# Performance work log

Measured on AMD Instinct MI355X. Metric: run time of the kernel, lower is better.

The kernel has to match this reference:

```python
import jax, jax.numpy as jnp
import numpy as np

N = 100000   # nodes
E = 1600000  # edges per view
B = 256      # graphs in batch
D = 128      # feature dim
H, C = 4, 32 # heads, per-head channels (H*C = 128)


def _seg_softmax(logits, seg, num_seg):
    # numerically stable softmax over segments (per-destination / per-graph)
    m = jax.ops.segment_max(logits, seg, num_segments=num_seg)
    e = jnp.exp(logits - m[seg])
    s = jax.ops.segment_sum(e, seg, num_segments=num_seg)
    return e / s[seg]


def _gat_conv(x, edge_index, W, att_src, att_dst, bias):
    # PyG GATConv with add_self_loops=True, concat heads
    n = x.shape[0]
    loop = jnp.arange(n, dtype=edge_index.dtype)
    src = jnp.concatenate([edge_index[0], loop])
    dst = jnp.concatenate([edge_index[1], loop])
    xh = (x @ W).reshape(n, H, C)                      # [N,H,C]
    a_src = jnp.einsum('nhc,hc->nh', xh, att_src)      # [N,H]
    a_dst = jnp.einsum('nhc,hc->nh', xh, att_dst)
    alpha = jax.nn.leaky_relu(a_src[src] + a_dst[dst], 0.2)   # [E+N,H]
    alpha = _seg_softmax(alpha, dst, n)
    msg = xh[src] * alpha[..., None]                   # [E+N,H,C]
    out = jax.ops.segment_sum(msg, dst, num_segments=n)
    return out.reshape(n, H * C) + bias


def _global_attention(h, batch, gate_W, gate_b):
    gate = (h @ gate_W + gate_b)[:, 0]                 # [N]
    a = _seg_softmax(gate, batch, B)
    return jax.ops.segment_sum(a[:, None] * h, batch, num_segments=B)  # [B,128]


def setup_inputs() -> dict:
    key = jax.random.key(0)
    ks = jax.random.split(key, 32)
    p = lambda k, shp: (jax.random.normal(k, shp, dtype=jnp.float32) * 0.05)
    inp = {
        'x': jax.random.normal(ks[0], (N, D), dtype=jnp.float32),
        'edge_index_ast': jax.random.randint(ks[1], (2, E), 0, N, dtype=jnp.int32),
        'edge_index_cfg': jax.random.randint(ks[2], (2, E), 0, N, dtype=jnp.int32),
        'edge_index_pdg': jax.random.randint(ks[3], (2, E), 0, N, dtype=jnp.int32),
        'batch': jnp.sort(jax.random.randint(ks[4], (N,), 0, B, dtype=jnp.int32)),
        'ln_g': jnp.ones((D,), jnp.float32),
        'ln_b': jnp.zeros((D,), jnp.float32),
        'proj_W': p(ks[5], (D, D)), 'proj_b': p(ks[6], (D,)),
        'W_ast': p(ks[7], (D, H * C)), 'att_src_ast': p(ks[8], (H, C)), 'att_dst_ast': p(ks[9], (H, C)), 'bias_ast': p(ks[10], (H * C,)),
        'W_cfg': p(ks[11], (D, H * C)), 'att_src_cfg': p(ks[12], (H, C)), 'att_dst_cfg': p(ks[13], (H, C)), 'bias_cfg': p(ks[14], (H * C,)),
        'W_pdg': p(ks[15], (D, H * C)), 'att_src_pdg': p(ks[16], (H, C)), 'att_dst_pdg': p(ks[17], (H, C)), 'bias_pdg': p(ks[18], (H * C,)),
        'gate_W': p(ks[19], (H * C, 1)), 'gate_b': p(ks[20], (1,)),
        'clf_W1': p(ks[21], (3 * H * C, 128)), 'clf_b1': p(ks[22], (128,)),
        'clf_W2': p(ks[23], (128, 1)), 'clf_b2': p(ks[24], (1,)),
    }
    return inp


def reference(x, edge_index_ast, edge_index_cfg, edge_index_pdg, batch,
              ln_g, ln_b, proj_W, proj_b,
              W_ast, att_src_ast, att_dst_ast, bias_ast,
              W_cfg, att_src_cfg, att_dst_cfg, bias_cfg,
              W_pdg, att_src_pdg, att_dst_pdg, bias_pdg,
              gate_W, gate_b, clf_W1, clf_b1, clf_W2, clf_b2):
    # LayerNorm + proj + LeakyReLU (dropout = eval/no-op)
    mu = jnp.mean(x, axis=-1, keepdims=True)
    var = jnp.var(x, axis=-1, keepdims=True)
    xn = (x - mu) * jax.lax.rsqrt(var + 1e-5) * ln_g + ln_b
    h0 = jax.nn.leaky_relu(xn @ proj_W + proj_b, 0.01)

    h_ast = jax.nn.elu(_gat_conv(h0, edge_index_ast, W_ast, att_src_ast, att_dst_ast, bias_ast))
    g_ast = _global_attention(h_ast, batch, gate_W, gate_b)
    h_cfg = jax.nn.elu(_gat_conv(h0, edge_index_cfg, W_cfg, att_src_cfg, att_dst_cfg, bias_cfg))
    g_cfg = _global_attention(h_cfg, batch, gate_W, gate_b)
    h_pdg = jax.nn.elu(_gat_conv(h0, edge_index_pdg, W_pdg, att_src_pdg, att_dst_pdg, bias_pdg))
    g_pdg = _global_attention(h_pdg, batch, gate_W, gate_b)

    combined = jnp.concatenate([g_ast, g_cfg, g_pdg], axis=1)  # [B, 384]
    hid = jax.nn.leaky_relu(combined @ clf_W1 + clf_b1, 0.01)
    return (hid @ clf_W2 + clf_b2).reshape(-1)                 # [B]
```

## Files before the change

### kernel.cpp

```cpp
#include <hip/hip_runtime.h>
#include <hip/hip_bf16.h>
#include <hip/hip_fp16.h>
#include <math.h>

#define NN 100000
#define EE 1600000
#define BB 256
#define NBUCK 391
#define PBLK 384
#define CH 4167
#define TOTB (3 * PBLK)
#define ROWS_PAD 100096
#define SCAP 4608
#define OBCAP (SCAP + 256)
#define LOG2E 1.442695041f
#define GEMM_BLKS 782
#define AGG_BLKS 25000
#define EPT 17
#define XH_ELEMS ((size_t)ROWS_PAD * 128)
#define A_ELEMS ((size_t)ROWS_PAD * 4)
#define HV_ELEMS ((size_t)NN * 128)

typedef short bf16x8 __attribute__((ext_vector_type(8)));
typedef float f32x4 __attribute__((ext_vector_type(4)));

__device__ __forceinline__ unsigned short f2bf(float f) {
    __hip_bfloat16 h = __float2bfloat16(f);
    return *(unsigned short*)&h;
}
__device__ __forceinline__ unsigned short f2h(float f) {
    __half h = __float2half(f);
    return *(unsigned short*)&h;
}
__device__ __forceinline__ float h2f(unsigned short u) {
    __half h = *(__half*)&u;
    return __half2float(h);
}

__global__ __launch_bounds__(256) void prep_kernel(const float* __restrict__ W0,
                                                   const float* __restrict__ W1,
                                                   const float* __restrict__ W2,
                                                   const float* __restrict__ W3,
                                                   const float* __restrict__ ln_g,
                                                   const float* __restrict__ ln_b,
                                                   unsigned short* __restrict__ WT,
                                                   float* __restrict__ c12,
                                                   int* __restrict__ counters) {
    if (blockIdx.x < 256) {
        int which = blockIdx.x >> 6;
        const float* W = which == 0 ? W0 : which == 1 ? W1 : which == 2 ? W2 : W3;
        int i = (blockIdx.x & 63) * 256 + threadIdx.x;
        int n = i >> 7, k = i & 127;
        float v = W[k * 128 + n];
        if (which == 0) v *= ln_g[k];
        WT[which * 16384 + i] = f2bf(v);
        return;
    }
    if (blockIdx.x == 257) {
        for (int i = threadIdx.x; i < 3 * NBUCK; i += 256) counters[i] = 0;
        return;
    }
    __shared__ float p1[256], p2[256];
    int t = threadIdx.x;
    int n = t & 127, kg = t >> 7;
    float c1 = 0.f, c2 = 0.f;
    for (int k = kg * 64; k < kg * 64 + 64; k++) {
        float w = W0[k * 128 + n];
        c1 = fmaf(ln_g[k], w, c1);
        c2 = fmaf(ln_b[k], w, c2);
    }
    p1[t] = c1; p2[t] = c2;
    __syncthreads();
    if (kg == 0) {
        c12[n] = p1[n] + p1[128 + n];
        c12[128 + n] = p2[n] + p2[128 + n];
    }
}


__device__ __forceinline__ void scatter_res_body(int bid, int tid,
                                                 const int* __restrict__ e0,
                                                 const int* __restrict__ e1,
                                                 const int* __restrict__ e2,
                                                 int* __restrict__ counters,
                                                 unsigned int* __restrict__ pairbuf) {
    int v = bid / PBLK, p = bid % PBLK;
    const int* ei = v == 0 ? e0 : v == 1 ? e1 : e2;
    __shared__ int hcnt[NBUCK];
    __shared__ int cur[NBUCK];
    for (int i = tid; i < NBUCK; i += 256) hcnt[i] = 0;
    __syncthreads();
    int ea = p * CH, ebnd = min(EE, ea + CH);
    unsigned val[EPT];
    int buck[EPT];
    #pragma unroll
    for (int k = 0; k < EPT; k++) {
        int e = ea + tid + k * 256;
        buck[k] = -1;
        val[k] = 0u;
        if (e < ebnd) {
            unsigned s = (unsigned)ei[e], d = (unsigned)ei[EE + e];
            val[k] = (s << 8) | (d & 255u);
            buck[k] = (int)(d >> 8);
        }
    }
    #pragma unroll
    for (int k = 0; k < EPT; k++)
        if (buck[k] >= 0) atomicAdd(&hcnt[buck[k]], 1);
    __syncthreads();
    int* gcnt = counters + v * NBUCK;
    for (int i = tid; i < NBUCK; i += 256) {
        int c = hcnt[i];
        cur[i] = c ? atomicAdd(&gcnt[i], c) : 0;
    }
    __syncthreads();
    unsigned int* pbuf = pairbuf + (size_t)v * NBUCK * SCAP;
    #pragma unroll
    for (int k = 0; k < EPT; k++) {
        if (buck[k] >= 0) {
            int pos = atomicAdd(&cur[buck[k]], 1);
            if (pos < SCAP) pbuf[(size_t)buck[k] * SCAP + pos] = val[k];
        }
    }
}

__device__ __forceinline__ void proj_body(int nb, int tid,
                                          const float* __restrict__ X,
                                          const unsigned short* __restrict__ WT,
                                          const float* __restrict__ c12,
                                          const float* __restrict__ pb,
                                          unsigned short* __restrict__ Out) {
    int w = tid >> 6, lane = tid & 63;
    int ln = lane & 15, oct = lane >> 4;
    int row0 = nb * 128 + w * 32;

    f32x4 acc[2][8];
    #pragma unroll
    for (int i = 0; i < 2; i++)
        #pragma unroll
        for (int j = 0; j < 8; j++) acc[i][j] = (f32x4){0.f, 0.f, 0.f, 0.f};

    const float* X0 = X + (size_t)min(row0 + ln, NN - 1) * 128;
    const float* X1 = X + (size_t)min(row0 + 16 + ln, NN - 1) * 128;
    const bf16x8* Wr = (const bf16x8*)(WT + (size_t)ln * 128);

    float s0 = 0.f, q0 = 0.f, s1 = 0.f, q1 = 0.f;
    #pragma unroll
    for (int kq = 0; kq < 4; kq++) {
        int koff = kq * 4 + oct;
        float4 xa = *(const float4*)(X0 + koff * 8);
        float4 xb = *(const float4*)(X0 + koff * 8 + 4);
        float4 ya = *(const float4*)(X1 + koff * 8);
        float4 yb = *(const float4*)(X1 + koff * 8 + 4);
        s0 += (xa.x + xa.y) + (xa.z + xa.w) + (xb.x + xb.y) + (xb.z + xb.w);
        q0 += xa.x * xa.x + xa.y * xa.y + xa.z * xa.z + xa.w * xa.w
            + xb.x * xb.x + xb.y * xb.y + xb.z * xb.z + xb.w * xb.w;
        s1 += (ya.x + ya.y) + (ya.z + ya.w) + (yb.x + yb.y) + (yb.z + yb.w);
        q1 += ya.x * ya.x + ya.y * ya.y + ya.z * ya.z + ya.w * ya.w
            + yb.x * yb.x + yb.y * yb.y + yb.z * yb.z + yb.w * yb.w;
        bf16x8 a0, a1;
        a0[0] = (short)f2bf(xa.x); a0[1] = (short)f2bf(xa.y); a0[2] = (short)f2bf(xa.z); a0[3] = (short)f2bf(xa.w);
        a0[4] = (short)f2bf(xb.x); a0[5] = (short)f2bf(xb.y); a0[6] = (short)f2bf(xb.z); a0[7] = (short)f2bf(xb.w);
        a1[0] = (short)f2bf(ya.x); a1[1] = (short)f2bf(ya.y); a1[2] = (short)f2bf(ya.z); a1[3] = (short)f2bf(ya.w);
        a1[4] = (short)f2bf(yb.x); a1[5] = (short)f2bf(yb.y); a1[6] = (short)f2bf(yb.z); a1[7] = (short)f2bf(yb.w);
        #pragma unroll
        for (int ct = 0; ct < 8; ct++) {
            bf16x8 bfr = Wr[ct * 16 * 16 + koff];
            acc[0][ct] = __builtin_amdgcn_mfma_f32_16x16x32_bf16(a0, bfr, acc[0][ct], 0, 0, 0);
            acc[1][ct] = __builtin_amdgcn_mfma_f32_16x16x32_bf16(a1, bfr, acc[1][ct], 0, 0, 0);
        }
    }
    #pragma unroll
    for (int m = 16; m < 64; m <<= 1) {
        s0 += __shfl_xor(s0, m); q0 += __shfl_xor(q0, m);
        s1 += __shfl_xor(s1, m); q1 += __shfl_xor(q1, m);
    }
    float mu0 = s0 * (1.0f / 128.0f);
    float rs0 = rsqrtf(q0 * (1.0f / 128.0f) - mu0 * mu0 + 1e-5f);
    float mu1 = s1 * (1.0f / 128.0f);
    float rs1 = rsqrtf(q1 * (1.0f / 128.0f) - mu1 * mu1 + 1e-5f);

    float c1v[8], c2v[8], pbv[8];
    #pragma unroll
    for (int ct = 0; ct < 8; ct++) {
        c1v[ct] = c12[ct * 16 + ln];
        c2v[ct] = c12[128 + ct * 16 + ln];
        pbv[ct] = pb[ct * 16 + ln];
    }
    #pragma unroll
    for (int rt = 0; rt < 2; rt++) {
        #pragma unroll
        for (int r = 0; r < 4; r++) {
            int src = oct * 4 + r;
            float rs_r = __shfl(rt ? rs1 : rs0, src);
            float mu_r = __shfl(rt ? mu1 : mu0, src);
            int row = row0 + rt * 16 + oct * 4 + r;
            #pragma unroll
            for (int ct = 0; ct < 8; ct++) {
                float v = rs_r * acc[rt][ct][r] - rs_r * mu_r * c1v[ct] + c2v[ct] + pbv[ct];
                v = v > 0.f ? v : 0.01f * v;
                Out[(size_t)row * 128 + ct * 16 + ln] = f2bf(v);
            }
        }
    }
}

__device__ __forceinline__ void view_body(int nb, int tid,
                                          const unsigned short* __restrict__ h0,
                                          const unsigned short* __restrict__ WTv,
                                          const float* __restrict__ asw,
                                          const float* __restrict__ adw,
                                          unsigned short* __restrict__ Out,
                                          float* __restrict__ a_src,
                                          float* __restrict__ a_dst) {
    int w = tid >> 6, lane = tid & 63;
    int ln = lane & 15, oct = lane >> 4;
    int row0 = nb * 128 + w * 32;

    f32x4 acc[2][8];
    #pragma unroll
    for (int i = 0; i < 2; i++)
        #pragma unroll
        for (int j = 0; j < 8; j++) acc[i][j] = (f32x4){0.f, 0.f, 0.f, 0.f};

    const bf16x8* Ar0 = (const bf16x8*)(h0 + (size_t)(row0 + ln) * 128);
    const bf16x8* Ar1 = (const bf16x8*)(h0 + (size_t)(row0 + 16 + ln) * 128);
    const bf16x8* Wr  = (const bf16x8*)(WTv + (size_t)ln * 128);

    #pragma unroll
    for (int kq = 0; kq < 4; kq++) {
        int koff = kq * 4 + oct;
        bf16x8 a0 = Ar0[koff];
        bf16x8 a1 = Ar1[koff];
        #pragma unroll
        for (int ct = 0; ct < 8; ct++) {
            bf16x8 bfr = Wr[ct * 16 * 16 + koff];
            acc[0][ct] = __builtin_amdgcn_mfma_f32_16x16x32_bf16(a0, bfr, acc[0][ct], 0, 0, 0);
            acc[1][ct] = __builtin_amdgcn_mfma_f32_16x16x32_bf16(a1, bfr, acc[1][ct], 0, 0, 0);
        }
    }
    float aswv[8], adwv[8];
    #pragma unroll
    for (int ct = 0; ct < 8; ct++) {
        aswv[ct] = asw[ct * 16 + ln] * LOG2E;
        adwv[ct] = adw[ct * 16 + ln] * LOG2E;
    }

    #pragma unroll
    for (int rt = 0; rt < 2; rt++) {
        #pragma unroll
        for (int r = 0; r < 4; r++) {
            int row = row0 + rt * 16 + oct * 4 + r;
            float sh_[4] = {0.f, 0.f, 0.f, 0.f}, dh_[4] = {0.f, 0.f, 0.f, 0.f};
            #pragma unroll
            for (int ct = 0; ct < 8; ct++) {
                float vv = acc[rt][ct][r];
                Out[(size_t)row * 128 + ct * 16 + ln] = f2h(vv);
                sh_[ct >> 1] = fmaf(vv, aswv[ct], sh_[ct >> 1]);
                dh_[ct >> 1] = fmaf(vv, adwv[ct], dh_[ct >> 1]);
            }
            #pragma unroll
            for (int off = 1; off < 16; off <<= 1) {
                #pragma unroll
                for (int h = 0; h < 4; h++) {
                    sh_[h] += __shfl_xor(sh_[h], off);
                    dh_[h] += __shfl_xor(dh_[h], off);
                }
            }
            if (ln == 0) {
                *(float4*)(a_src + (size_t)row * 4) = make_float4(sh_[0], sh_[1], sh_[2], sh_[3]);
                *(float4*)(a_dst + (size_t)row * 4) = make_float4(dh_[0], dh_[1], dh_[2], dh_[3]);
            }
        }
    }
}

__device__ __forceinline__ void fine_body(int bid, int t,
                                          const unsigned int* __restrict__ pairbuf,
                                          const int* __restrict__ counters,
                                          int* __restrict__ deg3,
                                          int* __restrict__ start3,
                                          unsigned int* __restrict__ ebuf3) {
    int v = bid / NBUCK, b = bid - v * NBUCK;
    int cnt = min(counters[v * NBUCK + b], SCAP);
    const unsigned int* pb = pairbuf + (size_t)(v * NBUCK + b) * SCAP;
    unsigned int* eb = ebuf3 + (size_t)(v * NBUCK + b) * OBCAP;
    int obase = (v * NBUCK + b) * OBCAP;
    __shared__ unsigned int slab[SCAP];
    __shared__ int hist[256], cur[256];
    __shared__ int wsum[4];
    int node = b * 256 + t;
    int valid = (node < NN) ? 1 : 0;
    hist[t] = valid;
    for (int i = t; i < cnt; i += 256) slab[i] = pb[i];
    __syncthreads();
    {
        int i = t;
        for (; i + 768 < cnt; i += 1024) {
            unsigned v0 = slab[i], v1 = slab[i + 256], v2 = slab[i + 512], v3 = slab[i + 768];
            atomicAdd(&hist[v0 & 255u], 1);
            atomicAdd(&hist[v1 & 255u], 1);
            atomicAdd(&hist[v2 & 255u], 1);
            atomicAdd(&hist[v3 & 255u], 1);
        }
        for (; i < cnt; i += 256) atomicAdd(&hist[slab[i] & 255u], 1);
    }
    __syncthreads();
    int hv = hist[t];
    int lanev = t & 63, wv = t >> 6;
    int incl = hv;
    #pragma unroll
    for (int m = 1; m < 64; m <<= 1) {
        int u = __shfl_up(incl, m);
        if (lanev >= m) incl += u;
    }
    if (lanev == 63) wsum[wv] = incl;
    __syncthreads();
    int prefix = 0;
    #pragma unroll
    for (int i = 0; i < 4; i++) prefix += (i < wv) ? wsum[i] : 0;
    int excl = incl + prefix - hv;
    cur[t] = excl + valid;
    if (valid) eb[excl] = (((unsigned)node) << 8) | ((unsigned)node & 255u);
    __syncthreads();
    {
        int i = t;
        for (; i + 768 < cnt; i += 1024) {
            unsigned v0 = slab[i], v1 = slab[i + 256], v2 = slab[i + 512], v3 = slab[i + 768];
            int p0 = atomicAdd(&cur[v0 & 255u], 1);
            int p1 = atomicAdd(&cur[v1 & 255u], 1);
            int p2 = atomicAdd(&cur[v2 & 255u], 1);
            int p3 = atomicAdd(&cur[v3 & 255u], 1);
            eb[p0] = v0; eb[p1] = v1; eb[p2] = v2; eb[p3] = v3;
        }
        for (; i < cnt; i += 256) {
            unsigned int val = slab[i];
            int pos = atomicAdd(&cur[val & 255u], 1);
            eb[pos] = val;
        }
    }
    if (valid) {
        deg3[v * NN + node] = hv;
        start3[v * NN + node] = obase + excl;
    }
}

__device__ __forceinline__ void agg_body(int node, int tid,
                                         const unsigned short* __restrict__ xh,
                                         const int* __restrict__ start,
                                         const int* __restrict__ deg,
                                         const unsigned int* __restrict__ ebuf,
                                         const float* __restrict__ a_src,
                                         const float* __restrict__ a_dst,
                                         const float* __restrict__ bias,
                                         const float* __restrict__ gw,
                                         const float* __restrict__ gb,
                                         unsigned short* __restrict__ hvb,
                                         float* __restrict__ gexpv,
                                         float* wlds) {
    int lane = tid & 63;
    int h = lane >> 4;
    int st = start[node];
    int cnt = deg[node];
    const char* xb = (const char*)xh;
    int laneoff = lane * 4;
    float4 ad4 = *(const float4*)(a_dst + (size_t)node * 4);
    float* ww = wlds + (tid >> 6) * 272;
    const float* wr = ww + h * 68;

    float accx = 0.f, accy = 0.f, den = 0.f;
    for (int j0 = 0; j0 < cnt; j0 += 64) {
        int nj = min(64, cnt - j0);
        int src_l = 0;
        if (lane < nj) {
            src_l = (int)(ebuf[st + j0 + lane] >> 8);
            float4 as4 = *(const float4*)(a_src + (size_t)src_l * 4);
            float t0 = as4.x + ad4.x, t1 = as4.y + ad4.y;
            float t2 = as4.z + ad4.z, t3 = as4.w + ad4.w;
            t0 = fmaxf(t0, 0.f) + 0.2f * fminf(t0, 0.f);
            t1 = fmaxf(t1, 0.f) + 0.2f * fminf(t1, 0.f);
            t2 = fmaxf(t2, 0.f) + 0.2f * fminf(t2, 0.f);
            t3 = fmaxf(t3, 0.f) + 0.2f * fminf(t3, 0.f);
            ww[0 * 68 + lane] = exp2f(t0);
            ww[1 * 68 + lane] = exp2f(t1);
            ww[2 * 68 + lane] = exp2f(t2);
            ww[3 * 68 + lane] = exp2f(t3);
        }
        int jj = 0;
        for (; jj + 8 <= nj; jj += 8) {
            int s0 = __builtin_amdgcn_readlane(src_l, jj);
            int s1 = __builtin_amdgcn_readlane(src_l, jj + 1);
            int s2 = __builtin_amdgcn_readlane(src_l, jj + 2);
            int s3 = __builtin_amdgcn_readlane(src_l, jj + 3);
            int s4 = __builtin_amdgcn_readlane(src_l, jj + 4);
            int s5 = __builtin_amdgcn_readlane(src_l, jj + 5);
            int s6 = __builtin_amdgcn_readlane(src_l, jj + 6);
            int s7 = __builtin_amdgcn_readlane(src_l, jj + 7);
            __half2 x0 = *(const __half2*)(xb + (((size_t)(unsigned)s0) << 8) + laneoff);
            __half2 x1 = *(const __half2*)(xb + (((size_t)(unsigned)s1) << 8) + laneoff);
            __half2 x2 = *(const __half2*)(xb + (((size_t)(unsigned)s2) << 8) + laneoff);
            __half2 x3 = *(const __half2*)(xb + (((size_t)(unsigned)s3) << 8) + laneoff);
            __half2 x4 = *(const __half2*)(xb + (((size_t)(unsigned)s4) << 8) + laneoff);
            __half2 x5 = *(const __half2*)(xb + (((size_t)(unsigned)s5) << 8) + laneoff);
            __half2 x6 = *(const __half2*)(xb + (((size_t)(unsigned)s6) << 8) + laneoff);
            __half2 x7 = *(const __half2*)(xb + (((size_t)(unsigned)s7) << 8) + laneoff);
            float4 wa = *(const float4*)(wr + jj);
            float4 wb = *(const float4*)(wr + jj + 4);
            den += (wa.x + wa.y) + (wa.z + wa.w) + (wb.x + wb.y) + (wb.z + wb.w);
            accx = fmaf(__low2float(x0), wa.x, accx);
            accy = fmaf(__high2float(x0), wa.x, accy);
            accx = fmaf(__low2float(x1), wa.y, accx);
            accy = fmaf(__high2float(x1), wa.y, accy);
            accx = fmaf(__low2float(x2), wa.z, accx);
            accy = fmaf(__high2float(x2), wa.z, accy);
            accx = fmaf(__low2float(x3), wa.w, accx);
            accy = fmaf(__high2float(x3), wa.w, accy);
            accx = fmaf(__low2float(x4), wb.x, accx);
            accy = fmaf(__high2float(x4), wb.x, accy);
            accx = fmaf(__low2float(x5), wb.y, accx);
            accy = fmaf(__high2float(x5), wb.y, accy);
            accx = fmaf(__low2float(x6), wb.z, accx);
            accy = fmaf(__high2float(x6), wb.z, accy);
            accx = fmaf(__low2float(x7), wb.w, accx);
            accy = fmaf(__high2float(x7), wb.w, accy);
        }
        for (; jj + 4 <= nj; jj += 4) {
            int s0 = __builtin_amdgcn_readlane(src_l, jj);
            int s1 = __builtin_amdgcn_readlane(src_l, jj + 1);
            int s2 = __builtin_amdgcn_readlane(src_l, jj + 2);
            int s3 = __builtin_amdgcn_readlane(src_l, jj + 3);
            __half2 x0 = *(const __half2*)(xb + (((size_t)(unsigned)s0) << 8) + laneoff);
            __half2 x1 = *(const __half2*)(xb + (((size_t)(unsigned)s1) << 8) + laneoff);
            __half2 x2 = *(const __half2*)(xb + (((size_t)(unsigned)s2) << 8) + laneoff);
            __half2 x3 = *(const __half2*)(xb + (((size_t)(unsigned)s3) << 8) + laneoff);
            float4 wa = *(const float4*)(wr + jj);
            den += (wa.x + wa.y) + (wa.z + wa.w);
            accx = fmaf(__low2float(x0), wa.x, accx);
            accy = fmaf(__high2float(x0), wa.x, accy);
            accx = fmaf(__low2float(x1), wa.y, accx);
            accy = fmaf(__high2float(x1), wa.y, accy);
            accx = fmaf(__low2float(x2), wa.z, accx);
            accy = fmaf(__high2float(x2), wa.z, accy);
            accx = fmaf(__low2float(x3), wa.w, accx);
            accy = fmaf(__high2float(x3), wa.w, accy);
        }
        for (; jj < nj; jj++) {
            int s = __builtin_amdgcn_readlane(src_l, jj);
            float w = wr[jj];
            __half2 xv = *(const __half2*)(xb + (((size_t)(unsigned)s) << 8) + laneoff);
            den += w;
            accx = fmaf(__low2float(xv), w, accx);
            accy = fmaf(__high2float(xv), w, accy);
        }
    }
    float inv = 1.0f / den;
    float2 bb = *(const float2*)(bias + lane * 2);
    float o0 = accx * inv + bb.x;
    float o1 = accy * inv + bb.y;
    o0 = o0 > 0.f ? o0 : exp2f(o0 * LOG2E) - 1.0f;
    o1 = o1 > 0.f ? o1 : exp2f(o1 * LOG2E) - 1.0f;
    unsigned int packed = (unsigned)f2h(o0) | ((unsigned)f2h(o1) << 16);
    *(unsigned int*)(hvb + (size_t)node * 128 + lane * 2) = packed;
    float2 g2 = *(const float2*)(gw + lane * 2);
    float gp = o0 * g2.x + o1 * g2.y;
    #pragma unroll
    for (int m = 1; m < 64; m <<= 1) gp += __shfl_xor(gp, m);
    if (lane == 0) gexpv[node] = exp2f((gp + gb[0]) * LOG2E);
}

__global__ __launch_bounds__(256) void fat_scatter_proj(const int* e0, const int* e1, const int* e2,
                                                        int* counters, unsigned int* pairbuf,
                                                        const float* X, const unsigned short* WT,
                                                        const float* c12, const float* pb,
                                                        unsigned short* h0) {
    if (blockIdx.x < TOTB) scatter_res_body(blockIdx.x, threadIdx.x, e0, e1, e2, counters, pairbuf);
    else proj_body(blockIdx.x - TOTB, threadIdx.x, X, WT, c12, pb, h0);
}

__global__ __launch_bounds__(256) void fat_fine_view3(const unsigned int* pairbuf, const int* counters,
                                                      int* deg3, int* start3, unsigned int* ebuf3,
                                                      const unsigned short* h0, const unsigned short* WT,
                                                      const float* as0, const float* ad0,
                                                      const float* as1, const float* ad1,
                                                      const float* as2, const float* ad2,
                                                      unsigned short* xh3, float* a_src3, float* a_dst3) {
    if (blockIdx.x < 3 * NBUCK) {
        fine_body(blockIdx.x, threadIdx.x, pairbuf, counters, deg3, start3, ebuf3);
        return;
    }
    int t = blockIdx.x - 3 * NBUCK;
    int v = t / GEMM_BLKS;
    int nb = t - v * GEMM_BLKS;
    const float* as_ = v == 0 ? as0 : v == 1 ? as1 : as2;
    const float* ad_ = v == 0 ? ad0 : v == 1 ? ad1 : ad2;
    view_body(nb, threadIdx.x, h0, WT + (size_t)(1 + v) * 16384, as_, ad_,
              xh3 + (size_t)v * XH_ELEMS,
              a_src3 + (size_t)v * A_ELEMS, a_dst3 + (size_t)v * A_ELEMS);
}

__global__ __launch_bounds__(256) void aggregate3_kernel(const unsigned short* __restrict__ xh3,
                                                         const int* __restrict__ start3,
                                                         const int* __restrict__ deg3,
                                                         const unsigned int* __restrict__ ebuf3,
                                                         const float* __restrict__ a_src3,
                                                         const float* __restrict__ a_dst3,
                                                         const float* __restrict__ b0,
                                                         const float* __restrict__ b1,
                                                         const float* __restrict__ b2,
                                                         const float* __restrict__ gw,
                                                         const float* __restrict__ gb,
                                                         unsigned short* __restrict__ hvb3,
                                                         float* __restrict__ gexpv3) {
    __shared__ float wlds[4 * 272];
    int v = blockIdx.x / AGG_BLKS;
    int bin = blockIdx.x - v * AGG_BLKS;
    int node = (bin * 256 + threadIdx.x) >> 6;
    if (node >= NN) return;
    const float* bias = v == 0 ? b0 : v == 1 ? b1 : b2;
    agg_body(node, threadIdx.x,
             xh3 + (size_t)v * XH_ELEMS,
             start3 + v * NN, deg3 + v * NN,
             ebuf3,
             a_src3 + (size_t)v * A_ELEMS, a_dst3 + (size_t)v * A_ELEMS,
             bias, gw, gb,
             hvb3 + (size_t)v * HV_ELEMS, gexpv3 + v * NN, wlds);
}

__global__ __launch_bounds__(1024) void pool_clf_kernel(const unsigned short* __restrict__ hvb3,
                                                        const float* __restrict__ gexpv3,
                                                        const int* __restrict__ batch,
                                                        const float* __restrict__ W1,
                                                        const float* __restrict__ b1,
                                                        const float* __restrict__ W2,
                                                        const float* __restrict__ b2,
                                                        float* __restrict__ out) {
    __shared__ float sacc[8 * 128];
    __shared__ float sws[8];
    __shared__ float gsh[384];
    __shared__ float sh[2];
    int b = blockIdx.x;
    int g = threadIdx.x >> 7;
    int ch = threadIdx.x & 127;
    int l = 0, r = NN;
    while (l < r) { int m = (l + r) >> 1; if (batch[m] < b) l = m + 1; else r = m; }
    int s0 = l;
    r = NN;
    while (l < r) { int m = (l + r) >> 1; if (batch[m] < b + 1) l = m + 1; else r = m; }
    int s1 = l;
    for (int v = 0; v < 3; v++) {
        const unsigned short* hvb = hvb3 + (size_t)v * HV_ELEMS;
        const float* gexpv = gexpv3 + v * NN;
        float acc = 0.f, wsum = 0.f;
        for (int n = s0 + g; n < s1; n += 8) {
            float w = gexpv[n];
            wsum += w;
            acc = fmaf(w, h2f(hvb[(size_t)n * 128 + ch]), acc);
        }
        sacc[g * 128 + ch] = acc;
        if (ch == 0) sws[g] = wsum;
        __syncthreads();
        if (g == 0) {
            float a = 0.f, w = 0.f;
            #pragma unroll
            for (int i = 0; i < 8; i++) { a += sacc[i * 128 + ch]; w += sws[i]; }
            gsh[v * 128 + ch] = (s1 > s0) ? a / w : 0.f;
        }
        __syncthreads();
    }
    if (threadIdx.x < 128) {
        int j = threadIdx.x;
        float acc = b1[j];
        for (int k = 0; k < 384; k++) acc = fmaf(gsh[k], W1[k * 128 + j], acc);
        acc = acc > 0.f ? acc : 0.01f * acc;
        float p = acc * W2[j];
        #pragma unroll
        for (int m = 1; m < 64; m <<= 1) p += __shfl_xor(p, m);
        if ((j & 63) == 0) sh[j >> 6] = p;
    }
    __syncthreads();
    if (threadIdx.x == 0) out[b] = sh[0] + sh[1] + b2[0];
}

extern "C" void kernel_launch(void* const* d_in, const int* in_sizes, int n_in,
                              void* d_out, int out_size, void* d_ws, size_t ws_size,
                              hipStream_t stream) {
    const float* x      = (const float*)d_in[0];
    const int*   ei[3]  = {(const int*)d_in[1], (const int*)d_in[2], (const int*)d_in[3]};
    const int*   batch  = (const int*)d_in[4];
    const float* ln_g   = (const float*)d_in[5];
    const float* ln_b   = (const float*)d_in[6];
    const float* proj_W = (const float*)d_in[7];
    const float* proj_b = (const float*)d_in[8];
    const float* Wv[3]  = {(const float*)d_in[9],  (const float*)d_in[13], (const float*)d_in[17]};
    const float* asv[3] = {(const float*)d_in[10], (const float*)d_in[14], (const float*)d_in[18]};
    const float* adv[3] = {(const float*)d_in[11], (const float*)d_in[15], (const float*)d_in[19]};
    const float* bv[3]  = {(const float*)d_in[12], (const float*)d_in[16], (const float*)d_in[20]};
    const float* gate_W = (const float*)d_in[21];
    const float* gate_b = (const float*)d_in[22];
    const float* clf_W1 = (const float*)d_in[23];
    const float* clf_b1 = (const float*)d_in[24];
    const float* clf_W2 = (const float*)d_in[25];
    const float* clf_b2 = (const float*)d_in[26];
    float* out = (float*)d_out;

    (void)in_sizes; (void)n_in; (void)out_size; (void)ws_size;

    char* base = (char*)d_ws;
    size_t off = 0;
    auto nxt = [&](size_t bytes) { char* r = base + off; off += (bytes + 255) & ~(size_t)255; return r; };

    unsigned short* h0   = (unsigned short*)nxt((size_t)ROWS_PAD * 128 * 2);
    unsigned short* xh3  = (unsigned short*)nxt((size_t)3 * XH_ELEMS * 2);
    unsigned short* hvb3 = (unsigned short*)nxt((size_t)3 * HV_ELEMS * 2);
    unsigned short* WT   = (unsigned short*)nxt(4 * 16384 * 2);
    float* c12    = (float*)nxt(256 * 4);
    float* a_src3 = (float*)nxt((size_t)3 * A_ELEMS * 4);
    float* a_dst3 = (float*)nxt((size_t)3 * A_ELEMS * 4);
    float* gexpv3 = (float*)nxt((size_t)3 * NN * 4);
    int* counters = (int*)nxt(3 * NBUCK * 4);
    int* deg3     = (int*)nxt(3 * NN * 4);
    int* start3   = (int*)nxt(3 * NN * 4);
    unsigned int* ebuf3   = (unsigned int*)nxt((size_t)3 * NBUCK * OBCAP * 4);
    unsigned int* pairbuf = (unsigned int*)nxt((size_t)3 * NBUCK * SCAP * 4);

    prep_kernel<<<258, 256, 0, stream>>>(proj_W, Wv[0], Wv[1], Wv[2], ln_g, ln_b, WT, c12, counters);
    fat_scatter_proj<<<TOTB + GEMM_BLKS, 256, 0, stream>>>(ei[0], ei[1], ei[2], counters, pairbuf,
                                                           x, WT, c12, proj_b, h0);
    fat_fine_view3<<<3 * NBUCK + 3 * GEMM_BLKS, 256, 0, stream>>>(
        pairbuf, counters, deg3, start3, ebuf3, h0, WT,
        asv[0], adv[0], asv[1], adv[1], asv[2], adv[2],
        xh3, a_src3, a_dst3);
    aggregate3_kernel<<<3 * AGG_BLKS, 256, 0, stream>>>(xh3, start3, deg3, ebuf3,
                                                        a_src3, a_dst3,
                                                        bv[0], bv[1], bv[2],
                                                        gate_W, gate_b, hvb3, gexpv3);
    pool_clf_kernel<<<256, 1024, 0, stream>>>(hvb3, gexpv3, batch,
                                              clf_W1, clf_b1, clf_W2, clf_b2, out);
}
```

Before: 587.9 us.

## Stagger per-view fine CSR build and pooling across aggregation kernels

The launch graph is restructured so that each view's fine bucket sort runs inside the kernel that aggregates the previous view. Pooling for views 0 and 1 is folded into the kernel that aggregates view 2, and only view 2's pooling and the classifier stay in the final kernel. The goal is to fill idle CUs and tail gaps by overlapping independent stages. The cost is more kernel launches, with pool blocks using 256 threads instead of 1024 (less parallelism per graph). Shared memory is now a single union buffer that both the fine and aggregation paths use.

```diff
diff --git a/kernel.cpp b/kernel.cpp
--- a/kernel.cpp
+++ b/kernel.cpp
@@ -17,6 +17,7 @@
 #define GEMM_BLKS 782
 #define AGG_BLKS 25000
 #define EPT 17
+#define SMEM_I (SCAP + 516)
 #define XH_ELEMS ((size_t)ROWS_PAD * 128)
 #define A_ELEMS ((size_t)ROWS_PAD * 4)
 #define HV_ELEMS ((size_t)NN * 128)
@@ -280,15 +281,17 @@
                                           const int* __restrict__ counters,
                                           int* __restrict__ deg3,
                                           int* __restrict__ start3,
-                                          unsigned int* __restrict__ ebuf3) {
+                                          unsigned int* __restrict__ ebuf3,
+                                          unsigned int* smem) {
     int v = bid / NBUCK, b = bid - v * NBUCK;
     int cnt = min(counters[v * NBUCK + b], SCAP);
     const unsigned int* pb = pairbuf + (size_t)(v * NBUCK + b) * SCAP;
     unsigned int* eb = ebuf3 + (size_t)(v * NBUCK + b) * OBCAP;
     int obase = (v * NBUCK + b) * OBCAP;
-    __shared__ unsigned int slab[SCAP];
-    __shared__ int hist[256], cur[256];
-    __shared__ int wsum[4];
+    unsigned int* slab = smem;
+    int* hist = (int*)(smem + SCAP);
+    int* cur  = hist + 256;
+    int* wsum = cur + 256;
     int node = b * 256 + t;
     int valid = (node < NN) ? 1 : 0;
     hist[t] = valid;
@@ -468,6 +471,36 @@
     if (lane == 0) gexpv[node] = exp2f((gp + gb[0]) * LOG2E);
 }
 
+__device__ __forceinline__ void pool256_body(int b, int tid,
+                                             const unsigned short* __restrict__ hvb,
+                                             const float* __restrict__ gexpv,
+                                             const int* __restrict__ batch,
+                                             float* dst,
+                                             float* sacc, float* sws) {
+    int g = tid >> 7;
+    int ch = tid & 127;
+    int l = 0, r = NN;
+    while (l < r) { int m = (l + r) >> 1; if (batch[m] < b) l = m + 1; else r = m; }
+    int s0 = l;
+    r = NN;
+    while (l < r) { int m = (l + r) >> 1; if (batch[m] < b + 1) l = m + 1; else r = m; }
+    int s1 = l;
+    float acc = 0.f, wsum = 0.f;
+    for (int n = s0 + g; n < s1; n += 2) {
+        float w = gexpv[n];
+        wsum += w;
+        acc = fmaf(w, h2f(hvb[(size_t)n * 128 + ch]), acc);
+    }
+    sacc[g * 128 + ch] = acc;
+    if (ch == 0) sws[g] = wsum;
+    __syncthreads();
+    if (g == 0) {
+        float a = sacc[ch] + sacc[128 + ch];
+        float w = sws[0] + sws[1];
+        dst[ch] = (s1 > s0) ? a / w : 0.f;
+    }
+}
+
 __global__ __launch_bounds__(256) void fat_scatter_proj(const int* e0, const int* e1, const int* e2,
                                                         int* counters, unsigned int* pairbuf,
                                                         const float* X, const unsigned short* WT,
@@ -477,18 +510,19 @@
     else proj_body(blockIdx.x - TOTB, threadIdx.x, X, WT, c12, pb, h0);
 }
 
-__global__ __launch_bounds__(256) void fat_fine_view3(const unsigned int* pairbuf, const int* counters,
-                                                      int* deg3, int* start3, unsigned int* ebuf3,
-                                                      const unsigned short* h0, const unsigned short* WT,
-                                                      const float* as0, const float* ad0,
-                                                      const float* as1, const float* ad1,
-                                                      const float* as2, const float* ad2,
-                                                      unsigned short* xh3, float* a_src3, float* a_dst3) {
-    if (blockIdx.x < 3 * NBUCK) {
-        fine_body(blockIdx.x, threadIdx.x, pairbuf, counters, deg3, start3, ebuf3);
+__global__ __launch_bounds__(256) void fat_fine0_view3(const unsigned int* pairbuf, const int* counters,
+                                                       int* deg3, int* start3, unsigned int* ebuf3,
+                                                       const unsigned short* h0, const unsigned short* WT,
+                                                       const float* as0, const float* ad0,
+                                                       const float* as1, const float* ad1,
+                                                       const float* as2, const float* ad2,
+                                                       unsigned short* xh3, float* a_src3, float* a_dst3) {
+    __shared__ unsigned int smem[SMEM_I];
+    if (blockIdx.x < NBUCK) {
+        fine_body(blockIdx.x, threadIdx.x, pairbuf, counters, deg3, start3, ebuf3, smem);
         return;
     }
-    int t = blockIdx.x - 3 * NBUCK;
+    int t = blockIdx.x - NBUCK;
     int v = t / GEMM_BLKS;
     int nb = t - v * GEMM_BLKS;
     const float* as_ = v == 0 ? as0 : v == 1 ? as1 : as2;
@@ -498,77 +532,79 @@
               a_src3 + (size_t)v * A_ELEMS, a_dst3 + (size_t)v * A_ELEMS);
 }
 
-__global__ __launch_bounds__(256) void aggregate3_kernel(const unsigned short* __restrict__ xh3,
-                                                         const int* __restrict__ start3,
-                                                         const int* __restrict__ deg3,
-                                                         const unsigned int* __restrict__ ebuf3,
-                                                         const float* __restrict__ a_src3,
-                                                         const float* __restrict__ a_dst3,
-                                                         const float* __restrict__ b0,
-                                                         const float* __restrict__ b1,
-                                                         const float* __restrict__ b2,
-                                                         const float* __restrict__ gw,
-                                                         const float* __restrict__ gb,
-                                                         unsigned short* __restrict__ hvb3,
-                                                         float* __restrict__ gexpv3) {
-    __shared__ float wlds[4 * 272];
-    int v = blockIdx.x / AGG_BLKS;
-    int bin = blockIdx.x - v * AGG_BLKS;
+__global__ __launch_bounds__(256) void fat_agg_fine(int vfine, int vagg,
+                                                    const unsigned int* pairbuf, const int* counters,
+                                                    int* deg3, int* start3, unsigned int* ebuf3,
+                                                    const unsigned short* xh3,
+                                                    const float* a_src3, const float* a_dst3,
+                                                    const float* b0, const float* b1, const float* b2,
+                                                    const float* gw, const float* gb,
+                                                    unsigned short* hvb3, float* gexpv3) {
+    __shared__ unsigned int smem[SMEM_I];
+    if (blockIdx.x < NBUCK) {
+        fine_body(vfine * NBUCK + blockIdx.x, threadIdx.x, pairbuf, counters, deg3, start3, ebuf3, smem);
+        return;
+    }
+    int bin = blockIdx.x - NBUCK;
     int node = (bin * 256 + threadIdx.x) >> 6;
     if (node >= NN) return;
-    const float* bias = v == 0 ? b0 : v == 1 ? b1 : b2;
+    const float* bias = vagg == 0 ? b0 : vagg == 1 ? b1 : b2;
     agg_body(node, threadIdx.x,
-             xh3 + (size_t)v * XH_ELEMS,
-             start3 + v * NN, deg3 + v * NN,
+             xh3 + (size_t)vagg * XH_ELEMS,
+             start3 + vagg * NN, deg3 + vagg * NN,
              ebuf3,
-             a_src3 + (size_t)v * A_ELEMS, a_dst3 + (size_t)v * A_ELEMS,
+             a_src3 + (size_t)vagg * A_ELEMS, a_dst3 + (size_t)vagg * A_ELEMS,
              bias, gw, gb,
-             hvb3 + (size_t)v * HV_ELEMS, gexpv3 + v * NN, wlds);
-}
-
-__global__ __launch_bounds__(1024) void pool_clf_kernel(const unsigned short* __restrict__ hvb3,
-                                                        const float* __restrict__ gexpv3,
-                                                        const int* __restrict__ batch,
-                                                        const float* __restrict__ W1,
-                                                        const float* __restrict__ b1,
-                                                        const float* __restrict__ W2,
-                                                        const float* __restrict__ b2,
-                                                        float* __restrict__ out) {
-    __shared__ float sacc[8 * 128];
-    __shared__ float sws[8];
+             hvb3 + (size_t)vagg * HV_ELEMS, gexpv3 + vagg * NN, (float*)smem);
+}
+
+__global__ __launch_bounds__(256) void fat_agg_pool(const unsigned short* xh3,
+                                                    const int* start3, const int* deg3,
+                                                    const unsigned int* ebuf3,
+                                                    const float* a_src3, const float* a_dst3,
+                                                    const float* b2v, const float* gw, const float* gb,
+                                                    unsigned short* hvb3, float* gexpv3,
+                                                    const int* batch, float* gout) {
+    __shared__ float fsm[1088];
+    if (blockIdx.x < 512) {
+        int v = blockIdx.x >> 8;
+        int b = blockIdx.x & 255;
+        pool256_body(b, threadIdx.x, hvb3 + (size_t)v * HV_ELEMS, gexpv3 + v * NN,
+                     batch, gout + b * 384 + v * 128, fsm, fsm + 256);
+        return;
+    }
+    int bin = blockIdx.x - 512;
+    int node = (bin * 256 + threadIdx.x) >> 6;
+    if (node >= NN) return;
+    agg_body(node, threadIdx.x,
+             xh3 + 2 * XH_ELEMS,
+             start3 + 2 * NN, deg3 + 2 * NN,
+             ebuf3,
+             a_src3 + 2 * A_ELEMS, a_dst3 + 2 * A_ELEMS,
+             b2v, gw, gb,
+             hvb3 + 2 * HV_ELEMS, gexpv3 + 2 * NN, fsm);
+}
+
+__global__ __launch_bounds__(256) void pool_clf_final(const unsigned short* __restrict__ hvb3,
+                                                      const float* __restrict__ gexpv3,
+                                                      const int* __restrict__ batch,
+                                                      const float* __restrict__ gout,
+                                                      const float* __restrict__ W1,
+                                                      const float* __restrict__ b1,
+                                                      const float* __restrict__ W2,
+                                                      const float* __restrict__ b2,
+                                                      float* __restrict__ out) {
+    __shared__ float sacc[256];
+    __shared__ float sws[2];
     __shared__ float gsh[384];
     __shared__ float sh[2];
     int b = blockIdx.x;
-    int g = threadIdx.x >> 7;
-    int ch = threadIdx.x & 127;
-    int l = 0, r = NN;
-    while (l < r) { int m = (l + r) >> 1; if (batch[m] < b) l = m + 1; else r = m; }
-    int s0 = l;
-    r = NN;
-    while (l < r) { int m = (l + r) >> 1; if (batch[m] < b + 1) l = m + 1; else r = m; }
-    int s1 = l;
-    for (int v = 0; v < 3; v++) {
-        const unsigned short* hvb = hvb3 + (size_t)v * HV_ELEMS;
-        const float* gexpv = gexpv3 + v * NN;
-        float acc = 0.f, wsum = 0.f;
-        for (int n = s0 + g; n < s1; n += 8) {
-            float w = gexpv[n];
-            wsum += w;
-            acc = fmaf(w, h2f(hvb[(size_t)n * 128 + ch]), acc);
-        }
-        sacc[g * 128 + ch] = acc;
-        if (ch == 0) sws[g] = wsum;
-        __syncthreads();
-        if (g == 0) {
-            float a = 0.f, w = 0.f;
-            #pragma unroll
-            for (int i = 0; i < 8; i++) { a += sacc[i * 128 + ch]; w += sws[i]; }
-            gsh[v * 128 + ch] = (s1 > s0) ? a / w : 0.f;
-        }
-        __syncthreads();
-    }
-    if (threadIdx.x < 128) {
-        int j = threadIdx.x;
+    int tid = threadIdx.x;
+    gsh[tid] = gout[b * 384 + tid];
+    pool256_body(b, tid, hvb3 + 2 * HV_ELEMS, gexpv3 + 2 * NN, batch, gsh + 256, sacc, sws);
+    __syncthreads();
+    if (tid < 128) {
+        int j = tid;
         float acc = b1[j];
         for (int k = 0; k < 384; k++) acc = fmaf(gsh[k], W1[k * 128 + j], acc);
         acc = acc > 0.f ? acc : 0.01f * acc;
@@ -578,7 +614,7 @@
         if ((j & 63) == 0) sh[j >> 6] = p;
     }
     __syncthreads();
-    if (threadIdx.x == 0) out[b] = sh[0] + sh[1] + b2[0];
+    if (tid == 0) out[b] = sh[0] + sh[1] + b2[0];
 }
 
 extern "C" void kernel_launch(void* const* d_in, const int* in_sizes, int n_in,
@@ -617,6 +653,7 @@
     float* a_src3 = (float*)nxt((size_t)3 * A_ELEMS * 4);
     float* a_dst3 = (float*)nxt((size_t)3 * A_ELEMS * 4);
     float* gexpv3 = (float*)nxt((size_t)3 * NN * 4);
+    float* gout   = (float*)nxt(BB * 384 * 4);
     int* counters = (int*)nxt(3 * NBUCK * 4);
     int* deg3     = (int*)nxt(3 * NN * 4);
     int* start3   = (int*)nxt(3 * NN * 4);
@@ -626,14 +663,24 @@
     prep_kernel<<<258, 256, 0, stream>>>(proj_W, Wv[0], Wv[1], Wv[2], ln_g, ln_b, WT, c12, counters);
     fat_scatter_proj<<<TOTB + GEMM_BLKS, 256, 0, stream>>>(ei[0], ei[1], ei[2], counters, pairbuf,
                                                            x, WT, c12, proj_b, h0);
-    fat_fine_view3<<<3 * NBUCK + 3 * GEMM_BLKS, 256, 0, stream>>>(
+    fat_fine0_view3<<<NBUCK + 3 * GEMM_BLKS, 256, 0, stream>>>(
         pairbuf, counters, deg3, start3, ebuf3, h0, WT,
         asv[0], adv[0], asv[1], adv[1], asv[2], adv[2],
         xh3, a_src3, a_dst3);
-    aggregate3_kernel<<<3 * AGG_BLKS, 256, 0, stream>>>(xh3, start3, deg3, ebuf3,
-                                                        a_src3, a_dst3,
-                                                        bv[0], bv[1], bv[2],
-                                                        gate_W, gate_b, hvb3, gexpv3);
-    pool_clf_kernel<<<256, 1024, 0, stream>>>(hvb3, gexpv3, batch,
-                                              clf_W1, clf_b1, clf_W2, clf_b2, out);
-}
+    fat_agg_fine<<<NBUCK + AGG_BLKS, 256, 0, stream>>>(1, 0, pairbuf, counters,
+                                                       deg3, start3, ebuf3,
+                                                       xh3, a_src3, a_dst3,
+                                                       bv[0], bv[1], bv[2], gate_W, gate_b,
+                                                       hvb3, gexpv3);
+    fat_agg_fine<<<NBUCK + AGG_BLKS, 256, 0, stream>>>(2, 1, pairbuf, counters,
+                                                       deg3, start3, ebuf3,
+                                                       xh3, a_src3, a_dst3,
+                                                       bv[0], bv[1], bv[2], gate_W, gate_b,
+                                                       hvb3, gexpv3);
+    fat_agg_pool<<<512 + AGG_BLKS, 256, 0, stream>>>(xh3, start3, deg3, ebuf3,
+                                                     a_src3, a_dst3,
+                                                     bv[2], gate_W, gate_b,
+                                                     hvb3, gexpv3, batch, gout);
+    pool_clf_final<<<256, 256, 0, stream>>>(hvb3, gexpv3, batch, gout,
+                                            clf_W1, clf_b1, clf_W2, clf_b2, out);
+}
```

Result: slower. 621.9 us (+5.8%).

## Aggregate two destination nodes per wavefront, packing their edge lists together

Applied to the files above, without the earlier changes.

Each 64-lane wavefront now handles two consecutive destination nodes and concatenates their edge lists into shared 64-wide chunks. Attention weights for both nodes are computed in one pass, and the gather-accumulate loop is split at the boundary between the two nodes. The aim is to fill more lanes in the per-chunk weight computation, since average degree is about 17, and to halve the number of wavefronts launched. The cost is more per-lane selects, the two-range loop with alignment handling, and a doubled epilogue per wave, which lengthens each wave's serial work.

```diff
diff --git a/kernel.cpp b/kernel.cpp
--- a/kernel.cpp
+++ b/kernel.cpp
@@ -15,7 +15,7 @@
 #define OBCAP (SCAP + 256)
 #define LOG2E 1.442695041f
 #define GEMM_BLKS 782
-#define AGG_BLKS 25000
+#define AGG2_BLKS 12500
 #define EPT 17
 #define XH_ELEMS ((size_t)ROWS_PAD * 128)
 #define A_ELEMS ((size_t)ROWS_PAD * 4)
@@ -345,114 +345,48 @@
     }
 }
 
-__device__ __forceinline__ void agg_body(int node, int tid,
-                                         const unsigned short* __restrict__ xh,
-                                         const int* __restrict__ start,
-                                         const int* __restrict__ deg,
-                                         const unsigned int* __restrict__ ebuf,
-                                         const float* __restrict__ a_src,
-                                         const float* __restrict__ a_dst,
-                                         const float* __restrict__ bias,
-                                         const float* __restrict__ gw,
-                                         const float* __restrict__ gb,
-                                         unsigned short* __restrict__ hvb,
-                                         float* __restrict__ gexpv,
-                                         float* wlds) {
-    int lane = tid & 63;
-    int h = lane >> 4;
-    int st = start[node];
-    int cnt = deg[node];
-    const char* xb = (const char*)xh;
-    int laneoff = lane * 4;
-    float4 ad4 = *(const float4*)(a_dst + (size_t)node * 4);
-    float* ww = wlds + (tid >> 6) * 272;
-    const float* wr = ww + h * 68;
-
-    float accx = 0.f, accy = 0.f, den = 0.f;
-    for (int j0 = 0; j0 < cnt; j0 += 64) {
-        int nj = min(64, cnt - j0);
-        int src_l = 0;
-        if (lane < nj) {
-            src_l = (int)(ebuf[st + j0 + lane] >> 8);
-            float4 as4 = *(const float4*)(a_src + (size_t)src_l * 4);
-            float t0 = as4.x + ad4.x, t1 = as4.y + ad4.y;
-            float t2 = as4.z + ad4.z, t3 = as4.w + ad4.w;
-            t0 = fmaxf(t0, 0.f) + 0.2f * fminf(t0, 0.f);
-            t1 = fmaxf(t1, 0.f) + 0.2f * fminf(t1, 0.f);
-            t2 = fmaxf(t2, 0.f) + 0.2f * fminf(t2, 0.f);
-            t3 = fmaxf(t3, 0.f) + 0.2f * fminf(t3, 0.f);
-            ww[0 * 68 + lane] = exp2f(t0);
-            ww[1 * 68 + lane] = exp2f(t1);
-            ww[2 * 68 + lane] = exp2f(t2);
-            ww[3 * 68 + lane] = exp2f(t3);
-        }
-        int jj = 0;
-        for (; jj + 8 <= nj; jj += 8) {
-            int s0 = __builtin_amdgcn_readlane(src_l, jj);
-            int s1 = __builtin_amdgcn_readlane(src_l, jj + 1);
-            int s2 = __builtin_amdgcn_readlane(src_l, jj + 2);
-            int s3 = __builtin_amdgcn_readlane(src_l, jj + 3);
-            int s4 = __builtin_amdgcn_readlane(src_l, jj + 4);
-            int s5 = __builtin_amdgcn_readlane(src_l, jj + 5);
-            int s6 = __builtin_amdgcn_readlane(src_l, jj + 6);
-            int s7 = __builtin_amdgcn_readlane(src_l, jj + 7);
-            __half2 x0 = *(const __half2*)(xb + (((size_t)(unsigned)s0) << 8) + laneoff);
-            __half2 x1 = *(const __half2*)(xb + (((size_t)(unsigned)s1) << 8) + laneoff);
-            __half2 x2 = *(const __half2*)(xb + (((size_t)(unsigned)s2) << 8) + laneoff);
-            __half2 x3 = *(const __half2*)(xb + (((size_t)(unsigned)s3) << 8) + laneoff);
-            __half2 x4 = *(const __half2*)(xb + (((size_t)(unsigned)s4) << 8) + laneoff);
-            __half2 x5 = *(const __half2*)(xb + (((size_t)(unsigned)s5) << 8) + laneoff);
-            __half2 x6 = *(const __half2*)(xb + (((size_t)(unsigned)s6) << 8) + laneoff);
-            __half2 x7 = *(const __half2*)(xb + (((size_t)(unsigned)s7) << 8) + laneoff);
-            float4 wa = *(const float4*)(wr + jj);
-            float4 wb = *(const float4*)(wr + jj + 4);
-            den += (wa.x + wa.y) + (wa.z + wa.w) + (wb.x + wb.y) + (wb.z + wb.w);
-            accx = fmaf(__low2float(x0), wa.x, accx);
-            accy = fmaf(__high2float(x0), wa.x, accy);
-            accx = fmaf(__low2float(x1), wa.y, accx);
-            accy = fmaf(__high2float(x1), wa.y, accy);
-            accx = fmaf(__low2float(x2), wa.z, accx);
-            accy = fmaf(__high2float(x2), wa.z, accy);
-            accx = fmaf(__low2float(x3), wa.w, accx);
-            accy = fmaf(__high2float(x3), wa.w, accy);
-            accx = fmaf(__low2float(x4), wb.x, accx);
-            accy = fmaf(__high2float(x4), wb.x, accy);
-            accx = fmaf(__low2float(x5), wb.y, accx);
-            accy = fmaf(__high2float(x5), wb.y, accy);
-            accx = fmaf(__low2float(x6), wb.z, accx);
-            accy = fmaf(__high2float(x6), wb.z, accy);
-            accx = fmaf(__low2float(x7), wb.w, accx);
-            accy = fmaf(__high2float(x7), wb.w, accy);
-        }
-        for (; jj + 4 <= nj; jj += 4) {
-            int s0 = __builtin_amdgcn_readlane(src_l, jj);
-            int s1 = __builtin_amdgcn_readlane(src_l, jj + 1);
-            int s2 = __builtin_amdgcn_readlane(src_l, jj + 2);
-            int s3 = __builtin_amdgcn_readlane(src_l, jj + 3);
-            __half2 x0 = *(const __half2*)(xb + (((size_t)(unsigned)s0) << 8) + laneoff);
-            __half2 x1 = *(const __half2*)(xb + (((size_t)(unsigned)s1) << 8) + laneoff);
-            __half2 x2 = *(const __half2*)(xb + (((size_t)(unsigned)s2) << 8) + laneoff);
-            __half2 x3 = *(const __half2*)(xb + (((size_t)(unsigned)s3) << 8) + laneoff);
-            float4 wa = *(const float4*)(wr + jj);
-            den += (wa.x + wa.y) + (wa.z + wa.w);
-            accx = fmaf(__low2float(x0), wa.x, accx);
-            accy = fmaf(__high2float(x0), wa.x, accy);
-            accx = fmaf(__low2float(x1), wa.y, accx);
-            accy = fmaf(__high2float(x1), wa.y, accy);
-            accx = fmaf(__low2float(x2), wa.z, accx);
-            accy = fmaf(__high2float(x2), wa.z, accy);
-            accx = fmaf(__low2float(x3), wa.w, accx);
-            accy = fmaf(__high2float(x3), wa.w, accy);
-        }
-        for (; jj < nj; jj++) {
-            int s = __builtin_amdgcn_readlane(src_l, jj);
-            float w = wr[jj];
-            __half2 xv = *(const __half2*)(xb + (((size_t)(unsigned)s) << 8) + laneoff);
-            den += w;
-            accx = fmaf(__low2float(xv), w, accx);
-            accy = fmaf(__high2float(xv), w, accy);
-        }
-    }
+#define AGG_SCALAR(JJ, AX, AY, DEN) { \
+        int s_ = __builtin_amdgcn_readlane(src_l, JJ); \
+        float w_ = wr[JJ]; \
+        __half2 xv_ = *(const __half2*)(xb + (((size_t)(unsigned)s_) << 8) + laneoff); \
+        DEN += w_; \
+        AX = fmaf(__low2float(xv_), w_, AX); \
+        AY = fmaf(__high2float(xv_), w_, AY); }
+
+#define AGG_QUAD(JJ, AX, AY, DEN) { \
+        int s0_ = __builtin_amdgcn_readlane(src_l, JJ); \
+        int s1_ = __builtin_amdgcn_readlane(src_l, (JJ) + 1); \
+        int s2_ = __builtin_amdgcn_readlane(src_l, (JJ) + 2); \
+        int s3_ = __builtin_amdgcn_readlane(src_l, (JJ) + 3); \
+        __half2 x0_ = *(const __half2*)(xb + (((size_t)(unsigned)s0_) << 8) + laneoff); \
+        __half2 x1_ = *(const __half2*)(xb + (((size_t)(unsigned)s1_) << 8) + laneoff); \
+        __half2 x2_ = *(const __half2*)(xb + (((size_t)(unsigned)s2_) << 8) + laneoff); \
+        __half2 x3_ = *(const __half2*)(xb + (((size_t)(unsigned)s3_) << 8) + laneoff); \
+        float4 wa_ = *(const float4*)(wr + (JJ)); \
+        DEN += (wa_.x + wa_.y) + (wa_.z + wa_.w); \
+        AX = fmaf(__low2float(x0_), wa_.x, AX); \
+        AY = fmaf(__high2float(x0_), wa_.x, AY); \
+        AX = fmaf(__low2float(x1_), wa_.y, AX); \
+        AY = fmaf(__high2float(x1_), wa_.y, AY); \
+        AX = fmaf(__low2float(x2_), wa_.z, AX); \
+        AY = fmaf(__high2float(x2_), wa_.z, AY); \
+        AX = fmaf(__low2float(x3_), wa_.w, AX); \
+        AY = fmaf(__high2float(x3_), wa_.w, AY); }
+
+#define AGG_RANGE(LO, HI, AX, AY, DEN) { \
+        int jj = (LO); \
+        for (; jj < (HI) && (jj & 3); jj++) AGG_SCALAR(jj, AX, AY, DEN) \
+        for (; jj + 8 <= (HI); jj += 8) { AGG_QUAD(jj, AX, AY, DEN) AGG_QUAD(jj + 4, AX, AY, DEN) } \
+        for (; jj + 4 <= (HI); jj += 4) AGG_QUAD(jj, AX, AY, DEN) \
+        for (; jj < (HI); jj++) AGG_SCALAR(jj, AX, AY, DEN) }
+
+__device__ __forceinline__ void agg_epilogue(int node, int lane,
+                                             float accx, float accy, float den,
+                                             const float* __restrict__ bias,
+                                             const float* __restrict__ gw,
+                                             const float* __restrict__ gb,
+                                             unsigned short* __restrict__ hvb,
+                                             float* __restrict__ gexpv) {
     float inv = 1.0f / den;
     float2 bb = *(const float2*)(bias + lane * 2);
     float o0 = accx * inv + bb.x;
@@ -466,6 +400,68 @@
     #pragma unroll
     for (int m = 1; m < 64; m <<= 1) gp += __shfl_xor(gp, m);
     if (lane == 0) gexpv[node] = exp2f((gp + gb[0]) * LOG2E);
+}
+
+__device__ __forceinline__ void agg2_body(int gid, int tid,
+                                          const unsigned short* __restrict__ xh,
+                                          const int* __restrict__ start,
+                                          const int* __restrict__ deg,
+                                          const unsigned int* __restrict__ ebuf,
+                                          const float* __restrict__ a_src,
+                                          const float* __restrict__ a_dst,
+                                          const float* __restrict__ bias,
+                                          const float* __restrict__ gw,
+                                          const float* __restrict__ gb,
+                                          unsigned short* __restrict__ hvb,
+                                          float* __restrict__ gexpv,
+                                          float* wlds) {
+    int nodeA = gid * 2;
+    int nodeB = nodeA + 1;
+    int lane = tid & 63;
+    int h = lane >> 4;
+    int stA = start[nodeA], cntA = deg[nodeA];
+    int stB = start[nodeB], cntB = deg[nodeB];
+    int total = cntA + cntB;
+    const char* xb = (const char*)xh;
+    int laneoff = lane * 4;
+    float4 adA = *(const float4*)(a_dst + (size_t)nodeA * 4);
+    float4 adB = *(const float4*)(a_dst + (size_t)nodeB * 4);
+    float* ww = wlds + (tid >> 6) * 272;
+    const float* wr = ww + h * 68;
+
+    float axA = 0.f, ayA = 0.f, dnA = 0.f;
+    float axB = 0.f, ayB = 0.f, dnB = 0.f;
+    for (int j0 = 0; j0 < total; j0 += 64) {
+        int nj = min(64, total - j0);
+        int src_l = 0;
+        if (lane < nj) {
+            int slot = j0 + lane;
+            int inA = slot < cntA;
+            int eidx = inA ? (stA + slot) : (stB + slot - cntA);
+            src_l = (int)(ebuf[eidx] >> 8);
+            float4 as4 = *(const float4*)(a_src + (size_t)(unsigned)src_l * 4);
+            float adx = inA ? adA.x : adB.x;
+            float ady = inA ? adA.y : adB.y;
+            float adz = inA ? adA.z : adB.z;
+            float adw = inA ? adA.w : adB.w;
+            float t0 = as4.x + adx, t1 = as4.y + ady;
+            float t2 = as4.z + adz, t3 = as4.w + adw;
+            t0 = fmaxf(t0, 0.f) + 0.2f * fminf(t0, 0.f);
+            t1 = fmaxf(t1, 0.f) + 0.2f * fminf(t1, 0.f);
+            t2 = fmaxf(t2, 0.f) + 0.2f * fminf(t2, 0.f);
+            t3 = fmaxf(t3, 0.f) + 0.2f * fminf(t3, 0.f);
+            ww[0 * 68 + lane] = exp2f(t0);
+            ww[1 * 68 + lane] = exp2f(t1);
+            ww[2 * 68 + lane] = exp2f(t2);
+            ww[3 * 68 + lane] = exp2f(t3);
+        }
+        int kA = cntA - j0;
+        kA = kA < 0 ? 0 : (kA > nj ? nj : kA);
+        AGG_RANGE(0, kA, axA, ayA, dnA)
+        AGG_RANGE(kA, nj, axB, ayB, dnB)
+    }
+    agg_epilogue(nodeA, lane, axA, ayA, dnA, bias, gw, gb, hvb, gexpv);
+    agg_epilogue(nodeB, lane, axB, ayB, dnB, bias, gw, gb, hvb, gexpv);
 }
 
 __global__ __launch_bounds__(256) void fat_scatter_proj(const int* e0, const int* e1, const int* e2,
@@ -512,18 +508,18 @@
                                                          unsigned short* __restrict__ hvb3,
                                                          float* __restrict__ gexpv3) {
     __shared__ float wlds[4 * 272];
-    int v = blockIdx.x / AGG_BLKS;
-    int bin = blockIdx.x - v * AGG_BLKS;
-    int node = (bin * 256 + threadIdx.x) >> 6;
-    if (node >= NN) return;
+    int v = blockIdx.x / AGG2_BLKS;
+    int bin = blockIdx.x - v * AGG2_BLKS;
+    int gid = bin * 4 + (threadIdx.x >> 6);
+    if (gid * 2 >= NN) return;
     const float* bias = v == 0 ? b0 : v == 1 ? b1 : b2;
-    agg_body(node, threadIdx.x,
-             xh3 + (size_t)v * XH_ELEMS,
-             start3 + v * NN, deg3 + v * NN,
-             ebuf3,
-             a_src3 + (size_t)v * A_ELEMS, a_dst3 + (size_t)v * A_ELEMS,
-             bias, gw, gb,
-             hvb3 + (size_t)v * HV_ELEMS, gexpv3 + v * NN, wlds);
+    agg2_body(gid, threadIdx.x,
+              xh3 + (size_t)v * XH_ELEMS,
+              start3 + v * NN, deg3 + v * NN,
+              ebuf3,
+              a_src3 + (size_t)v * A_ELEMS, a_dst3 + (size_t)v * A_ELEMS,
+              bias, gw, gb,
+              hvb3 + (size_t)v * HV_ELEMS, gexpv3 + v * NN, wlds);
 }
 
 __global__ __launch_bounds__(1024) void pool_clf_kernel(const unsigned short* __restrict__ hvb3,
@@ -630,10 +626,10 @@
         pairbuf, counters, deg3, start3, ebuf3, h0, WT,
         asv[0], adv[0], asv[1], adv[1], asv[2], adv[2],
         xh3, a_src3, a_dst3);
-    aggregate3_kernel<<<3 * AGG_BLKS, 256, 0, stream>>>(xh3, start3, deg3, ebuf3,
-                                                        a_src3, a_dst3,
-                                                        bv[0], bv[1], bv[2],
-                                                        gate_W, gate_b, hvb3, gexpv3);
+    aggregate3_kernel<<<3 * AGG2_BLKS, 256, 0, stream>>>(xh3, start3, deg3, ebuf3,
+                                                         a_src3, a_dst3,
+                                                         bv[0], bv[1], bv[2],
+                                                         gate_W, gate_b, hvb3, gexpv3);
     pool_clf_kernel<<<256, 1024, 0, stream>>>(hvb3, gexpv3, batch,
                                               clf_W1, clf_b1, clf_W2, clf_b2, out);
 }
```

After: 574.1 us. 2.3% less time.
